# Kernel tuning notes

Hardware: AMD Instinct MI355X
Metric: run time of the kernel (lower is better)

The kernel has to match this reference:

```python
import jax, jax.numpy as jnp
import numpy as np

T, NNODES, DEG = 32, 10000, 32
IN_DIM, H1, HEADS, H2, GRU, PH = 128, 32, 4, 32, 32, 5


def setup_inputs() -> dict:
    key = jax.random.key(0)
    ks = jax.random.split(key, 24)
    d = {}
    d["h"] = jax.random.normal(ks[0], (T, NNODES, IN_DIM), jnp.float32)
    d["src"] = jax.random.randint(ks[1], (NNODES, DEG), 0, NNODES, dtype=jnp.int32)
    d["N"] = jnp.ones((1,), jnp.float32)
    d["I"] = jax.random.uniform(ks[2], (T,), jnp.float32)
    d["R"] = jax.random.uniform(ks[3], (T,), jnp.float32)
    d["S"] = jax.random.uniform(ks[4], (T,), jnp.float32)
    d["It"] = jax.random.uniform(ks[5], (T,), jnp.float32)
    d["Rt"] = jax.random.uniform(ks[6], (T,), jnp.float32)
    d["hx0"] = jax.random.normal(ks[7], (1, GRU), jnp.float32)
    # layer1: HEADS independent GATLayers (fc no-bias, attn_fc no-bias)
    d["W1"] = jax.random.normal(ks[8], (HEADS, IN_DIM, H1), jnp.float32) / np.sqrt(IN_DIM)
    d["a1"] = jax.random.normal(ks[9], (HEADS, 2 * H1), jnp.float32) / np.sqrt(2 * H1)
    # layer2: single head over concatenated features
    d["W2"] = jax.random.normal(ks[10], (1, HEADS * H1, H2), jnp.float32) / np.sqrt(HEADS * H1)
    d["a2"] = jax.random.normal(ks[11], (1, 2 * H2), jnp.float32) / np.sqrt(2 * H2)
    # GRUCell params (torch layout: W_ih [3*gru, in], W_hh [3*gru, gru])
    sg = 1.0 / np.sqrt(GRU)
    d["W_ih"] = jax.random.normal(ks[12], (3 * GRU, H2), jnp.float32) * sg
    d["W_hh"] = jax.random.normal(ks[13], (3 * GRU, GRU), jnp.float32) * sg
    d["b_ih"] = jax.random.normal(ks[14], (3 * GRU,), jnp.float32) * sg
    d["b_hh"] = jax.random.normal(ks[15], (3 * GRU,), jnp.float32) * sg
    sr = 1.0 / np.sqrt(GRU + 2)
    d["Wr1"] = jax.random.normal(ks[16], (2 * PH, GRU + 2), jnp.float32) * sr
    d["br1"] = jax.random.normal(ks[17], (2 * PH,), jnp.float32) * sr
    d["Wr2"] = jax.random.normal(ks[18], (2, GRU + 2), jnp.float32) * sr
    d["br2"] = jax.random.normal(ks[19], (2,), jnp.float32) * sr
    return d


def _gat(x, W, a, src):
    # x: [n, din]; W: [H, din, dout]; a: [H, 2*dout]; src: [n, D] in-neighbor ids
    dout = W.shape[-1]
    z = jnp.einsum('nd,hde->hne', x, W)                    # [H, n, dout]
    zs = z[:, src]                                          # [H, n, D, dout] mailbox of src feats
    e = (jnp.einsum('hnde,he->hnd', zs, a[:, :dout])        # a . z_src part
         + jnp.einsum('hne,he->hn', z, a[:, dout:])[:, :, None])  # a . z_dst part
    alpha = jax.nn.softmax(jax.nn.leaky_relu(e, 0.01), axis=-1)   # softmax over mailbox dim
    return jnp.einsum('hnd,hnde->hne', alpha, zs)           # [H, n, dout]


def reference(h, src, N, I, R, S, It, Rt, hx0, W1, a1, W2, a2,
              W_ih, W_hh, b_ih, b_hh, Wr1, br1, Wr2, br2):
    n = h.shape[1]
    Ns = N.squeeze()

    def step(hx, xs):
        iz, I_t, R_t, S_t, It_t, Rt_t = xs
        h1 = jax.nn.relu(_gat(iz, W1, a1, src))             # [H, n, H1]
        h1 = jnp.transpose(h1, (1, 0, 2)).reshape(n, -1)    # cat heads -> [n, H*H1]
        h2 = _gat(h1, W2, a2, src)[0]                       # [n, H2]
        cur = jnp.max(jax.nn.relu(h2), axis=0)[None, :]     # [1, H2]
        # GRUCell
        gi = cur @ W_ih.T + b_ih
        gh = hx @ W_hh.T + b_hh
        gir, giz, gin = jnp.split(gi, 3, axis=1)
        ghr, ghz, ghn = jnp.split(gh, 3, axis=1)
        r = jax.nn.sigmoid(gir + ghr)
        zg = jax.nn.sigmoid(giz + ghz)
        ng = jnp.tanh(gin + r * ghn)
        hx_new = (1.0 - zg) * ng + zg * hx                  # [1, GRU]
        new_hx = jnp.concatenate([hx_new, It_t.reshape(1, 1), Rt_t.reshape(1, 1)], axis=1)
        pred = (new_hx @ Wr1.T + br1).squeeze()             # [2*PH]
        ab = (new_hx @ Wr2.T + br2).squeeze()               # [2]
        a_s = jax.nn.sigmoid(ab[0])
        b_s = jax.nn.sigmoid(ab[1])
        new_I_t = pred[0::2]
        new_R_t = pred[1::2]
        # SIR physics rollout with detached recurrence
        last_I, last_R, last_S = I_t, R_t, S_t
        phyI, phyR = [], []
        dI = jnp.zeros(())
        dR = jnp.zeros(())
        for i in range(PH):
            if i > 0:
                last_I = last_I + jax.lax.stop_gradient(dI)
                last_R = last_R + jax.lax.stop_gradient(dR)
                last_S = Ns - last_I - last_R
            dI = a_s * last_I * (last_S / Ns) - b_s * last_I
            dR = b_s * last_I
            phyI.append(dI)
            phyR.append(dR)
        return hx_new, (new_I_t, new_R_t, jnp.stack(phyI), jnp.stack(phyR))

    _, (nI, nR, pI, pR) = jax.lax.scan(step, hx0, (h, I, R, S, It, Rt))
    return nI, nR, pI.reshape(-1), pR.reshape(-1)
```

## Files before the change

### kernel.cpp

```cpp
#include <hip/hip_runtime.h>

typedef __attribute__((ext_vector_type(8))) short short8;
typedef __attribute__((ext_vector_type(4))) float floatx4;
typedef __attribute__((ext_vector_type(2))) float float2v;
typedef __attribute__((ext_vector_type(4))) unsigned int uint4v;
typedef __attribute__((ext_vector_type(4))) int int4v;
typedef __attribute__((ext_vector_type(2))) unsigned int uint2v;

__device__ __forceinline__ float bf2f(unsigned short u) {
    return __uint_as_float(((unsigned int)u) << 16);
}
__device__ __forceinline__ unsigned short f2bf(float f) {
    unsigned int x = __float_as_uint(f);
    unsigned int r = (x + 0x7FFFu + ((x >> 16) & 1u)) >> 16;
    return (unsigned short)r;
}
__device__ __forceinline__ float ldf(const void* p, long i, bool f32) {
    return f32 ? ((const float*)p)[i] : bf2f(((const unsigned short*)p)[i]);
}
__device__ __forceinline__ bool detect_f32(const unsigned short* Nv) {
    return Nv[0] == 0;
}

#define P_WIH 0
#define P_WHH 3072
#define P_BIH 6144
#define P_BHH 6240
#define P_WR1 6336
#define P_BR1 6676
#define P_WR2 6686
#define P_BR2 6754
#define P_I   6756
#define P_R   6788
#define P_S   6820
#define P_IT  6852
#define P_RT  6884
#define P_N   6916
#define P_HX0 6917
#define P_TOT 6949

__global__ __launch_bounds__(256) void norm_params(
    const void* W1, const void* a1, const void* W2, const void* a2,
    const void* W_ih, const void* W_hh, const void* b_ih, const void* b_hh,
    const void* Wr1, const void* br1, const void* Wr2, const void* br2,
    const void* Iv, const void* Rv, const void* Sv, const void* Itv, const void* Rtv,
    const void* Nv, const void* hx0,
    float* __restrict__ P, unsigned short* __restrict__ WbT1,
    unsigned short* __restrict__ WbT2)
{
    bool f32 = detect_f32((const unsigned short*)Nv);
    int tid = threadIdx.x;
    struct Item { const void* p; int n; int off; };
    const Item items[15] = {
        {W_ih, 3072, P_WIH}, {W_hh, 3072, P_WHH}, {b_ih, 96, P_BIH}, {b_hh, 96, P_BHH},
        {Wr1, 340, P_WR1}, {br1, 10, P_BR1}, {Wr2, 68, P_WR2}, {br2, 2, P_BR2},
        {Iv, 32, P_I}, {Rv, 32, P_R}, {Sv, 32, P_S}, {Itv, 32, P_IT}, {Rtv, 32, P_RT},
        {Nv, 1, P_N}, {hx0, 32, P_HX0}
    };
    for (int it = 0; it < 15; it++)
        for (int i = tid; i < items[it].n; i += 256)
            P[items[it].off + i] = ldf(items[it].p, i, f32);

    for (int idx = tid; idx < 144 * 128; idx += 256) {
        int col = idx >> 7, k = idx & 127;
        float v = 0.f;
        if (col < 128) {
            int h = col >> 5, e = col & 31;
            v = ldf(W1, (h * 128 + k) * 32 + e, f32);
        } else if (col < 136) {
            int q = col - 128;
            int h = (q < 4) ? q : q - 4;
            int off = (q < 4) ? 0 : 32;
            float s = 0.f;
            for (int e = 0; e < 32; e++)
                s += ldf(W1, (h * 128 + k) * 32 + e, f32) * ldf(a1, h * 64 + off + e, f32);
            v = s;
        }
        WbT1[col * 128 + k] = f2bf(v);
    }
    for (int idx = tid; idx < 48 * 128; idx += 256) {
        int col = idx >> 7, k = idx & 127;
        float v = 0.f;
        if (col < 32) {
            v = ldf(W2, k * 32 + col, f32);
        } else if (col < 34) {
            int off = (col == 32) ? 0 : 32;
            float s = 0.f;
            for (int e = 0; e < 32; e++)
                s += ldf(W2, k * 32 + e, f32) * ldf(a2, off + e, f32);
            v = s;
        }
        WbT2[col * 128 + k] = f2bf(v);
    }
}

template<int NT, int HC, bool DYN>
__global__ __launch_bounds__(256) void gat_linear(
    const void* __restrict__ Xv, const unsigned short* __restrict__ WbT,
    unsigned short* __restrict__ Z, float* __restrict__ EL, float* __restrict__ ER,
    const unsigned short* __restrict__ Nv, long row0)
{
    constexpr int NCOL = NT * 16;
    constexpr int LDW  = 136;
    __shared__ unsigned short Ws[NCOL * LDW];
    int tid = threadIdx.x;
    for (int idx = tid; idx < NCOL * 16; idx += 256) {
        int col = idx >> 4, ch = idx & 15;
        *(uint4v*)(&Ws[col * LDW + ch * 8]) = *(const uint4v*)(&WbT[col * 128 + ch * 8]);
    }
    __syncthreads();

    bool f32 = DYN ? detect_f32(Nv) : false;
    int wave = tid >> 6, lane = tid & 63;
    int l15 = lane & 15, quad = lane >> 4;
    long lrow = (long)blockIdx.x * 64 + wave * 16;

    floatx4 acc[NT];
    floatx4 zz = {0.f, 0.f, 0.f, 0.f};
    #pragma unroll
    for (int i = 0; i < NT; i++) acc[i] = zz;

    long xoff = (row0 + lrow + l15) * 128 + quad * 8;
    #pragma unroll
    for (int kt = 0; kt < 4; kt++) {
        short8 afrag;
        if (DYN && f32) {
            const float* xr = (const float*)Xv + xoff + kt * 32;
            float4 u0 = ((const float4*)xr)[0];
            float4 u1 = ((const float4*)xr)[1];
            union { short8 v; unsigned short u[8]; } af;
            af.u[0] = f2bf(u0.x); af.u[1] = f2bf(u0.y);
            af.u[2] = f2bf(u0.z); af.u[3] = f2bf(u0.w);
            af.u[4] = f2bf(u1.x); af.u[5] = f2bf(u1.y);
            af.u[6] = f2bf(u1.z); af.u[7] = f2bf(u1.w);
            afrag = af.v;
        } else {
            afrag = *(const short8*)((const unsigned short*)Xv + xoff + kt * 32);
        }
        #pragma unroll
        for (int nt = 0; nt < NT; nt++) {
            short8 bfrag = *(const short8*)(&Ws[(nt * 16 + l15) * LDW + kt * 32 + quad * 8]);
            acc[nt] = __builtin_amdgcn_mfma_f32_16x16x32_bf16(afrag, bfrag, acc[nt], 0, 0, 0);
        }
    }

    #pragma unroll
    for (int nt = 0; nt < NT; nt++) {
        int col = nt * 16 + l15;
        #pragma unroll
        for (int r = 0; r < 4; r++) {
            long grow = lrow + quad * 4 + r;
            float v = acc[nt][r];
            if (col < HC * 32) {
                Z[grow * (HC * 32) + col] = f2bf(v);
            } else if (col < HC * 32 + HC) {
                EL[grow * HC + (col - HC * 32)] = v;
            } else if (col < HC * 32 + 2 * HC) {
                ER[grow * HC + (col - HC * 32 - HC)] = v;
            }
        }
    }
}

__global__ __launch_bounds__(256, 3) void gat1_aggr(
    const int* __restrict__ src,
    const unsigned short* __restrict__ Z,
    const float* __restrict__ EL,
    const float* __restrict__ ER,
    unsigned short* __restrict__ H1,
    int NX)
{
    __shared__ float als[4][8][4][36];
    __shared__ int   sid[4][8][32];
    int tid = threadIdx.x;
    int w = tid >> 6, lane = tid & 63;
    int d31 = lane & 31, g = lane >> 5;
    int fl = lane & 15, q = lane >> 4;
    int h = fl >> 2;

    int bid = blockIdx.x;
    int xcd = bid % NX;
    int j   = bid / NX;
    int tq  = j / 313;
    int r   = j - tq * 313;
    int t   = tq * NX + xcd;
    int tb  = t * 10000;
    int n0  = r * 32 + w * 8;
    const char* Zb = (const char*)Z + (size_t)tb * 256;

    int sidx[8];
    float2v elv[8], erv[8];
    #pragma unroll
    for (int jj = 0; jj < 8; jj++) {
        int n = n0 + jj; n = n > 9999 ? 9999 : n;
        sidx[jj] = src[n * 32 + d31];
    }
    #pragma unroll
    for (int jj = 0; jj < 8; jj++)
        elv[jj] = *(const float2v*)(EL + (size_t)(tb + sidx[jj]) * 4 + g * 2);
    #pragma unroll
    for (int jj = 0; jj < 8; jj++) {
        int n = n0 + jj; n = n > 9999 ? 9999 : n;
        erv[jj] = *(const float2v*)(ER + (size_t)(tb + n) * 4 + g * 2);
    }
    float e0[8], e1[8], m0[8], m1[8];
    #pragma unroll
    for (int jj = 0; jj < 8; jj++) {
        float a = elv[jj][0] + erv[jj][0];
        float b = elv[jj][1] + erv[jj][1];
        e0[jj] = a >= 0.f ? a : 0.01f * a;
        e1[jj] = b >= 0.f ? b : 0.01f * b;
        m0[jj] = e0[jj]; m1[jj] = e1[jj];
    }
    #pragma unroll
    for (int off = 16; off > 0; off >>= 1) {
        #pragma unroll
        for (int jj = 0; jj < 8; jj++) {
            m0[jj] = fmaxf(m0[jj], __shfl_xor(m0[jj], off));
            m1[jj] = fmaxf(m1[jj], __shfl_xor(m1[jj], off));
        }
    }
    float x0[8], x1[8], s0[8], s1[8];
    #pragma unroll
    for (int jj = 0; jj < 8; jj++) {
        x0[jj] = __expf(e0[jj] - m0[jj]);
        x1[jj] = __expf(e1[jj] - m1[jj]);
        s0[jj] = x0[jj]; s1[jj] = x1[jj];
    }
    #pragma unroll
    for (int off = 16; off > 0; off >>= 1) {
        #pragma unroll
        for (int jj = 0; jj < 8; jj++) {
            s0[jj] += __shfl_xor(s0[jj], off);
            s1[jj] += __shfl_xor(s1[jj], off);
        }
    }
    #pragma unroll
    for (int jj = 0; jj < 8; jj++) {
        als[w][jj][2 * g + 0][d31] = x0[jj] / s0[jj];
        als[w][jj][2 * g + 1][d31] = x1[jj] / s1[jj];
        if (g == 0) sid[w][jj][d31] = sidx[jj];
    }
    __builtin_amdgcn_wave_barrier();

    uint4v buf[2][8];
    {
        int4v ia = *(const int4v*)&sid[w][0][q * 8];
        int4v ib = *(const int4v*)&sid[w][0][q * 8 + 4];
        #pragma unroll
        for (int k = 0; k < 4; k++)
            buf[0][k] = *(const uint4v*)(Zb + (unsigned int)(ia[k] * 256 + fl * 16));
        #pragma unroll
        for (int k = 0; k < 4; k++)
            buf[0][4 + k] = *(const uint4v*)(Zb + (unsigned int)(ib[k] * 256 + fl * 16));
    }
    #pragma unroll
    for (int jj = 0; jj < 8; jj++) {
        int pb = jj & 1;
        if (jj < 7) {
            int4v ia = *(const int4v*)&sid[w][jj + 1][q * 8];
            int4v ib = *(const int4v*)&sid[w][jj + 1][q * 8 + 4];
            #pragma unroll
            for (int k = 0; k < 4; k++)
                buf[pb ^ 1][k] = *(const uint4v*)(Zb + (unsigned int)(ia[k] * 256 + fl * 16));
            #pragma unroll
            for (int k = 0; k < 4; k++)
                buf[pb ^ 1][4 + k] = *(const uint4v*)(Zb + (unsigned int)(ib[k] * 256 + fl * 16));
        }
        floatx4 avA = *(const floatx4*)&als[w][jj][h][q * 8];
        floatx4 avB = *(const floatx4*)&als[w][jj][h][q * 8 + 4];
        float2v c[4];
        #pragma unroll
        for (int i = 0; i < 4; i++) c[i] = (float2v){0.f, 0.f};
        #pragma unroll
        for (int k = 0; k < 8; k++) {
            float a = (k < 4) ? avA[k & 3] : avB[k & 3];
            float2v a2 = {a, a};
            uint4v ld = buf[pb][k];
            float2v f0 = {__uint_as_float(ld.x << 16), __uint_as_float(ld.x & 0xffff0000u)};
            float2v f1 = {__uint_as_float(ld.y << 16), __uint_as_float(ld.y & 0xffff0000u)};
            float2v f2 = {__uint_as_float(ld.z << 16), __uint_as_float(ld.z & 0xffff0000u)};
            float2v f3 = {__uint_as_float(ld.w << 16), __uint_as_float(ld.w & 0xffff0000u)};
            c[0] += a2 * f0;
            c[1] += a2 * f1;
            c[2] += a2 * f2;
            c[3] += a2 * f3;
        }
        #pragma unroll
        for (int i = 0; i < 4; i++) {
            c[i][0] += __shfl_xor(c[i][0], 16);
            c[i][1] += __shfl_xor(c[i][1], 16);
            c[i][0] += __shfl_xor(c[i][0], 32);
            c[i][1] += __shfl_xor(c[i][1], 32);
        }
        if (q == 0 && n0 + jj < 10000) {
            uint4v o;
            #pragma unroll
            for (int i = 0; i < 4; i++) {
                float lo = fmaxf(c[i][0], 0.f);
                float hi = fmaxf(c[i][1], 0.f);
                o[i] = (unsigned int)f2bf(lo) | ((unsigned int)f2bf(hi) << 16);
            }
            __builtin_nontemporal_store(o,
                (uint4v*)((char*)H1 + (size_t)(tb + n0 + jj) * 256 + fl * 16));
        }
    }
}

__global__ __launch_bounds__(256, 4) void gat2_aggr(
    const int* __restrict__ src,
    const unsigned short* __restrict__ Z2,
    const float* __restrict__ EL2,
    const float* __restrict__ ER2,
    int* __restrict__ cur, int t0, int NX)
{
    __shared__ float als2[4][8][32];
    __shared__ int bm[32];
    int tid = threadIdx.x, w = tid >> 6, lane = tid & 63;
    int d31 = lane & 31, g = lane >> 5;
    int g3 = lane >> 3, f7 = lane & 7;

    int bid = blockIdx.x;
    int xcd = bid % NX;
    int j   = bid / NX;
    int tq  = j / 157;
    int r   = j - tq * 157;
    int t   = tq * NX + xcd;
    int tb  = t * 10000;
    int n0  = r * 64 + w * 16;
    const char* Zb = (const char*)Z2 + (size_t)tb * 64;

    if (tid < 32) bm[tid] = 0;
    __syncthreads();

    float m4[4] = {0.f, 0.f, 0.f, 0.f};
    #pragma unroll
    for (int b = 0; b < 2; b++) {
        int nb = n0 + b * 8;
        float ev[8];
        #pragma unroll
        for (int jj = 0; jj < 8; jj++) {
            int n = nb + jj;
            bool ok = n < 10000;
            int sidx = ok ? src[n * 32 + d31] : 0;
            float e = ok ? (EL2[tb + sidx] + ER2[tb + n]) : 0.f;
            ev[jj] = e >= 0.f ? e : 0.01f * e;
        }
        float mx[8];
        #pragma unroll
        for (int jj = 0; jj < 8; jj++) mx[jj] = ev[jj];
        #pragma unroll
        for (int off = 16; off > 0; off >>= 1) {
            #pragma unroll
            for (int jj = 0; jj < 8; jj++)
                mx[jj] = fmaxf(mx[jj], __shfl_xor(mx[jj], off));
        }
        float xv[8], sm[8];
        #pragma unroll
        for (int jj = 0; jj < 8; jj++) { xv[jj] = __expf(ev[jj] - mx[jj]); sm[jj] = xv[jj]; }
        #pragma unroll
        for (int off = 16; off > 0; off >>= 1) {
            #pragma unroll
            for (int jj = 0; jj < 8; jj++)
                sm[jj] += __shfl_xor(sm[jj], off);
        }
        if (g == 0) {
            #pragma unroll
            for (int jj = 0; jj < 8; jj++)
                als2[w][jj][d31] = xv[jj] / sm[jj];
        }
        __builtin_amdgcn_wave_barrier();

        #pragma unroll
        for (int jj = 0; jj < 8; jj++) {
            int n = nb + jj;
            if (n >= 10000) continue;
            floatx4 av4 = *(const floatx4*)&als2[w][jj][g3 * 4];
            int4v mv = *(const int4v*)(src + n * 32 + g3 * 4);
            uint2v ldv[4];
            #pragma unroll
            for (int k = 0; k < 4; k++)
                ldv[k] = *(const uint2v*)(Zb + (unsigned int)(mv[k] * 64 + f7 * 8));
            float c0 = 0.f, c1 = 0.f, c2 = 0.f, c3 = 0.f;
            #pragma unroll
            for (int k = 0; k < 4; k++) {
                c0 += av4[k] * __uint_as_float(ldv[k].x << 16);
                c1 += av4[k] * __uint_as_float(ldv[k].x & 0xffff0000u);
                c2 += av4[k] * __uint_as_float(ldv[k].y << 16);
                c3 += av4[k] * __uint_as_float(ldv[k].y & 0xffff0000u);
            }
            #pragma unroll
            for (int off = 8; off <= 32; off <<= 1) {
                c0 += __shfl_xor(c0, off);
                c1 += __shfl_xor(c1, off);
                c2 += __shfl_xor(c2, off);
                c3 += __shfl_xor(c3, off);
            }
            m4[0] = fmaxf(m4[0], c0);
            m4[1] = fmaxf(m4[1], c1);
            m4[2] = fmaxf(m4[2], c2);
            m4[3] = fmaxf(m4[3], c3);
        }
        __builtin_amdgcn_wave_barrier();
    }
    if (lane < 8) {
        #pragma unroll
        for (int i = 0; i < 4; i++)
            atomicMax(&bm[f7 * 4 + i], __float_as_int(m4[i]));
    }
    __syncthreads();
    if (tid < 32) atomicMax(&cur[(t0 + t) * 32 + tid], bm[tid]);
}

__global__ __launch_bounds__(128) void gru_head(
    const float* __restrict__ P, const float* __restrict__ cur,
    void* __restrict__ outv, const unsigned short* __restrict__ Nv)
{
    bool f32 = detect_f32(Nv);
    __shared__ float Whh[96 * 32], giAll[32 * 96];
    __shared__ float hx[32], gh[96], nh[34];
    int tid = threadIdx.x;
    for (int i = tid; i < 96 * 32; i += 128)
        Whh[i] = P[P_WHH + i];
    for (int o = tid; o < 32 * 96; o += 128) {
        int t = o / 96, gg = o - t * 96;
        float s = P[P_BIH + gg];
        for (int k = 0; k < 32; k++)
            s += cur[t * 32 + k] * P[P_WIH + gg * 32 + k];
        giAll[o] = s;
    }
    if (tid < 32) hx[tid] = P[P_HX0 + tid];
    __syncthreads();

    for (int t = 0; t < 32; t++) {
        if (tid < 96) {
            float sh = 0.f;
            for (int k = 0; k < 32; k++)
                sh += hx[k] * Whh[tid * 32 + k];
            gh[tid] = sh + P[P_BHH + tid];
        }
        __syncthreads();
        if (tid < 32) {
            const float* gi = &giAll[t * 96];
            float r  = 1.f / (1.f + __expf(-(gi[tid] + gh[tid])));
            float zg = 1.f / (1.f + __expf(-(gi[32 + tid] + gh[32 + tid])));
            float ng = tanhf(gi[64 + tid] + r * gh[64 + tid]);
            float hv = (1.f - zg) * ng + zg * hx[tid];
            hx[tid] = hv;
            nh[tid] = hv;
            if (tid == 0) { nh[32] = P[P_IT + t]; nh[33] = P[P_RT + t]; }
        }
        __syncthreads();
        if (tid < 10) {
            float s = P[P_BR1 + tid];
            for (int k = 0; k < 34; k++) s += nh[k] * P[P_WR1 + tid * 34 + k];
            int i = tid >> 1;
            int oi = ((tid & 1) == 0) ? (t * 5 + i) : (160 + t * 5 + i);
            if (f32) ((float*)outv)[oi] = s;
            else     ((unsigned short*)outv)[oi] = f2bf(s);
        }
        if (tid == 64) {
            float ab0 = P[P_BR2 + 0], ab1 = P[P_BR2 + 1];
            for (int k = 0; k < 34; k++) {
                ab0 += nh[k] * P[P_WR2 + k];
                ab1 += nh[k] * P[P_WR2 + 34 + k];
            }
            float a_s = 1.f / (1.f + __expf(-ab0));
            float b_s = 1.f / (1.f + __expf(-ab1));
            float Ns = P[P_N];
            float lI = P[P_I + t], lR = P[P_R + t], lS = P[P_S + t];
            float dI = 0.f, dR = 0.f;
            for (int i = 0; i < 5; i++) {
                if (i > 0) { lI += dI; lR += dR; lS = Ns - lI - lR; }
                dI = a_s * lI * (lS / Ns) - b_s * lI;
                dR = b_s * lI;
                if (f32) {
                    ((float*)outv)[320 + t * 5 + i] = dI;
                    ((float*)outv)[480 + t * 5 + i] = dR;
                } else {
                    ((unsigned short*)outv)[320 + t * 5 + i] = f2bf(dI);
                    ((unsigned short*)outv)[480 + t * 5 + i] = f2bf(dR);
                }
            }
        }
        __syncthreads();
    }
}

extern "C" void kernel_launch(void* const* d_in, const int* in_sizes, int n_in,
                              void* d_out, int out_size, void* d_ws, size_t ws_size,
                              hipStream_t stream) {
    const void* h    = d_in[0];
    const int*  src  = (const int*)d_in[1];
    const void* Nv   = d_in[2];
    const void* Iv   = d_in[3];
    const void* Rv   = d_in[4];
    const void* Sv   = d_in[5];
    const void* Itv  = d_in[6];
    const void* Rtv  = d_in[7];
    const void* hx0  = d_in[8];
    const void* W1   = d_in[9];
    const void* a1   = d_in[10];
    const void* W2   = d_in[11];
    const void* a2   = d_in[12];
    const void* W_ih = d_in[13];
    const void* W_hh = d_in[14];
    const void* b_ih = d_in[15];
    const void* b_hh = d_in[16];
    const void* Wr1  = d_in[17];
    const void* br1  = d_in[18];
    const void* Wr2  = d_in[19];
    const void* br2  = d_in[20];
    const unsigned short* Nu = (const unsigned short*)Nv;

    int TC = 4;
    for (int c = 32; c >= 4; c >>= 1) {
        size_t need = (size_t)c * 10000 * (128 * 2 + 128 * 2 + 16 + 16) + (1 << 20);
        if (need <= ws_size) { TC = c; break; }
    }
    long CR = (long)TC * 10000;

    char* ws = (char*)d_ws;
    size_t off = 0;
    auto alloc = [&](size_t b) {
        void* p = ws + off;
        off += (b + 255) & ~(size_t)255;
        return p;
    };
    float*          Pb   = (float*)alloc(P_TOT * 4);
    unsigned short* WbT1 = (unsigned short*)alloc(144 * 128 * 2);
    unsigned short* WbT2 = (unsigned short*)alloc(48 * 128 * 2);
    float*          cur  = (float*)alloc(32 * 32 * 4);
    unsigned short* z1   = (unsigned short*)alloc((size_t)CR * 128 * 2);
    unsigned short* h1   = (unsigned short*)alloc((size_t)CR * 128 * 2);
    float*          el1  = (float*)alloc((size_t)CR * 4 * 4);
    float*          er1  = (float*)alloc((size_t)CR * 4 * 4);
    unsigned short* z2   = z1;
    float*          el2  = el1;
    float*          er2  = er1;

    (void)hipMemsetAsync(cur, 0, 32 * 32 * 4, stream);
    norm_params<<<1, 256, 0, stream>>>(W1, a1, W2, a2, W_ih, W_hh, b_ih, b_hh,
                                       Wr1, br1, Wr2, br2, Iv, Rv, Sv, Itv, Rtv,
                                       Nv, hx0, Pb, WbT1, WbT2);
    int nchunks = 32 / TC;
    int g1 = (int)(CR / 64);
    int NX = TC < 8 ? TC : 8;
    int TQ = TC / NX;
    for (int c = 0; c < nchunks; c++) {
        long row0 = (long)c * CR;
        gat_linear<9, 4, true><<<g1, 256, 0, stream>>>(h, WbT1, z1, el1, er1, Nu, row0);
        gat1_aggr<<<NX * 313 * TQ, 256, 0, stream>>>(src, z1, el1, er1, h1, NX);
        gat_linear<3, 1, false><<<g1, 256, 0, stream>>>(h1, WbT2, z2, el2, er2, Nu, 0);
        gat2_aggr<<<NX * 157 * TQ, 256, 0, stream>>>(src, z2, el2, er2, (int*)cur, c * TC, NX);
    }
    gru_head<<<1, 128, 0, stream>>>(Pb, cur, d_out, Nu);
}
```

Measured before the change: 688.5 us.

## Remap gat1 aggregation to one node per lane group and use DPP reductions

The gat1 aggregation is remapped so each 16-lane group owns one destination node and walks all 32 neighbours itself. This removes the per-node cross-lane shuffle reduction, and the gathers are issued in two alternating batches of eight loads. Softmax max/sum reductions in both GAT aggregation kernels move from shfl_xor to DPP row rotations plus ds_swizzle, and divisions become hardware reciprocals. Output packing uses the native v_cvt_pk_bf16_f32 instruction. The cost is higher register pressure from holding all neighbour ids and weights per lane, and the reciprocal is slightly less accurate.

```diff
diff --git a/kernel.cpp b/kernel.cpp
--- a/kernel.cpp
+++ b/kernel.cpp
@@ -21,6 +21,35 @@
 __device__ __forceinline__ bool detect_f32(const unsigned short* Nv) {
     return Nv[0] == 0;
 }
+
+template<int CTRL>
+__device__ __forceinline__ float dppf(float x) {
+    return __int_as_float(__builtin_amdgcn_update_dpp(
+        0, __float_as_int(x), CTRL, 0xF, 0xF, true));
+}
+__device__ __forceinline__ float swz16(float x) {
+    return __int_as_float(__builtin_amdgcn_ds_swizzle(__float_as_int(x), 0x401F));
+}
+__device__ __forceinline__ float red32max(float x) {
+    x = fmaxf(x, dppf<0x128>(x));
+    x = fmaxf(x, dppf<0x124>(x));
+    x = fmaxf(x, dppf<0x122>(x));
+    x = fmaxf(x, dppf<0x121>(x));
+    return fmaxf(x, swz16(x));
+}
+__device__ __forceinline__ float red32sum(float x) {
+    x += dppf<0x128>(x);
+    x += dppf<0x124>(x);
+    x += dppf<0x122>(x);
+    x += dppf<0x121>(x);
+    return x + swz16(x);
+}
+__device__ __forceinline__ float addx8_dpp(float x) {
+    return x + dppf<0x128>(x);
+}
+
+#define BFLO(u) __uint_as_float((u) << 16)
+#define BFHI(u) __uint_as_float((u) & 0xffff0000u)
 
 #define P_WIH 0
 #define P_WHH 3072
@@ -162,6 +191,29 @@
     }
 }
 
+__device__ __forceinline__ void iss8(uint4v* buf, const int4v sa, const int4v sb,
+                                     const char* Zb, unsigned fb) {
+    #pragma unroll
+    for (int k = 0; k < 4; k++)
+        buf[k] = *(const uint4v*)(Zb + (unsigned)(sa[k] * 256) + fb);
+    #pragma unroll
+    for (int k = 0; k < 4; k++)
+        buf[4 + k] = *(const uint4v*)(Zb + (unsigned)(sb[k] * 256) + fb);
+}
+__device__ __forceinline__ void cons8(const uint4v* buf, const floatx4 ax, const floatx4 ay,
+                                      float2v& c0, float2v& c1, float2v& c2, float2v& c3) {
+    #pragma unroll
+    for (int k = 0; k < 8; k++) {
+        float a = (k < 4) ? ax[k & 3] : ay[k & 3];
+        float2v ap = {a, a};
+        uint4v ld = buf[k];
+        c0 += ap * (float2v){BFLO(ld.x), BFHI(ld.x)};
+        c1 += ap * (float2v){BFLO(ld.y), BFHI(ld.y)};
+        c2 += ap * (float2v){BFLO(ld.z), BFHI(ld.z)};
+        c3 += ap * (float2v){BFLO(ld.w), BFHI(ld.w)};
+    }
+}
+
 __global__ __launch_bounds__(256, 3) void gat1_aggr(
     const int* __restrict__ src,
     const unsigned short* __restrict__ Z,
@@ -175,8 +227,6 @@
     int tid = threadIdx.x;
     int w = tid >> 6, lane = tid & 63;
     int d31 = lane & 31, g = lane >> 5;
-    int fl = lane & 15, q = lane >> 4;
-    int h = fl >> 2;
 
     int bid = blockIdx.x;
     int xcd = bid % NX;
@@ -203,106 +253,84 @@
         int n = n0 + jj; n = n > 9999 ? 9999 : n;
         erv[jj] = *(const float2v*)(ER + (size_t)(tb + n) * 4 + g * 2);
     }
-    float e0[8], e1[8], m0[8], m1[8];
+    float e0[8], e1[8];
     #pragma unroll
     for (int jj = 0; jj < 8; jj++) {
         float a = elv[jj][0] + erv[jj][0];
         float b = elv[jj][1] + erv[jj][1];
         e0[jj] = a >= 0.f ? a : 0.01f * a;
         e1[jj] = b >= 0.f ? b : 0.01f * b;
-        m0[jj] = e0[jj]; m1[jj] = e1[jj];
-    }
-    #pragma unroll
-    for (int off = 16; off > 0; off >>= 1) {
-        #pragma unroll
-        for (int jj = 0; jj < 8; jj++) {
-            m0[jj] = fmaxf(m0[jj], __shfl_xor(m0[jj], off));
-            m1[jj] = fmaxf(m1[jj], __shfl_xor(m1[jj], off));
-        }
-    }
-    float x0[8], x1[8], s0[8], s1[8];
+    }
+    float x0[8], x1[8];
     #pragma unroll
     for (int jj = 0; jj < 8; jj++) {
-        x0[jj] = __expf(e0[jj] - m0[jj]);
-        x1[jj] = __expf(e1[jj] - m1[jj]);
-        s0[jj] = x0[jj]; s1[jj] = x1[jj];
-    }
-    #pragma unroll
-    for (int off = 16; off > 0; off >>= 1) {
-        #pragma unroll
-        for (int jj = 0; jj < 8; jj++) {
-            s0[jj] += __shfl_xor(s0[jj], off);
-            s1[jj] += __shfl_xor(s1[jj], off);
-        }
+        x0[jj] = __expf(e0[jj] - red32max(e0[jj]));
+        x1[jj] = __expf(e1[jj] - red32max(e1[jj]));
     }
     #pragma unroll
     for (int jj = 0; jj < 8; jj++) {
-        als[w][jj][2 * g + 0][d31] = x0[jj] / s0[jj];
-        als[w][jj][2 * g + 1][d31] = x1[jj] / s1[jj];
+        float r0 = __builtin_amdgcn_rcpf(red32sum(x0[jj]));
+        float r1 = __builtin_amdgcn_rcpf(red32sum(x1[jj]));
+        als[w][jj][2 * g + 0][d31] = x0[jj] * r0;
+        als[w][jj][2 * g + 1][d31] = x1[jj] * r1;
         if (g == 0) sid[w][jj][d31] = sidx[jj];
     }
     __builtin_amdgcn_wave_barrier();
 
-    uint4v buf[2][8];
-    {
-        int4v ia = *(const int4v*)&sid[w][0][q * 8];
-        int4v ib = *(const int4v*)&sid[w][0][q * 8 + 4];
-        #pragma unroll
-        for (int k = 0; k < 4; k++)
-            buf[0][k] = *(const uint4v*)(Zb + (unsigned int)(ia[k] * 256 + fl * 16));
-        #pragma unroll
-        for (int k = 0; k < 4; k++)
-            buf[0][4 + k] = *(const uint4v*)(Zb + (unsigned int)(ib[k] * 256 + fl * 16));
-    }
-    #pragma unroll
-    for (int jj = 0; jj < 8; jj++) {
-        int pb = jj & 1;
-        if (jj < 7) {
-            int4v ia = *(const int4v*)&sid[w][jj + 1][q * 8];
-            int4v ib = *(const int4v*)&sid[w][jj + 1][q * 8 + 4];
-            #pragma unroll
-            for (int k = 0; k < 4; k++)
-                buf[pb ^ 1][k] = *(const uint4v*)(Zb + (unsigned int)(ia[k] * 256 + fl * 16));
-            #pragma unroll
-            for (int k = 0; k < 4; k++)
-                buf[pb ^ 1][4 + k] = *(const uint4v*)(Zb + (unsigned int)(ib[k] * 256 + fl * 16));
-        }
-        floatx4 avA = *(const floatx4*)&als[w][jj][h][q * 8];
-        floatx4 avB = *(const floatx4*)&als[w][jj][h][q * 8 + 4];
-        float2v c[4];
-        #pragma unroll
-        for (int i = 0; i < 4; i++) c[i] = (float2v){0.f, 0.f};
-        #pragma unroll
-        for (int k = 0; k < 8; k++) {
-            float a = (k < 4) ? avA[k & 3] : avB[k & 3];
-            float2v a2 = {a, a};
-            uint4v ld = buf[pb][k];
-            float2v f0 = {__uint_as_float(ld.x << 16), __uint_as_float(ld.x & 0xffff0000u)};
-            float2v f1 = {__uint_as_float(ld.y << 16), __uint_as_float(ld.y & 0xffff0000u)};
-            float2v f2 = {__uint_as_float(ld.z << 16), __uint_as_float(ld.z & 0xffff0000u)};
-            float2v f3 = {__uint_as_float(ld.w << 16), __uint_as_float(ld.w & 0xffff0000u)};
-            c[0] += a2 * f0;
-            c[1] += a2 * f1;
-            c[2] += a2 * f2;
-            c[3] += a2 * f3;
-        }
-        #pragma unroll
-        for (int i = 0; i < 4; i++) {
-            c[i][0] += __shfl_xor(c[i][0], 16);
-            c[i][1] += __shfl_xor(c[i][1], 16);
-            c[i][0] += __shfl_xor(c[i][0], 32);
-            c[i][1] += __shfl_xor(c[i][1], 32);
-        }
-        if (q == 0 && n0 + jj < 10000) {
-            uint4v o;
-            #pragma unroll
-            for (int i = 0; i < 4; i++) {
-                float lo = fmaxf(c[i][0], 0.f);
-                float hi = fmaxf(c[i][1], 0.f);
-                o[i] = (unsigned int)f2bf(lo) | ((unsigned int)f2bf(hi) << 16);
-            }
+    int u = lane >> 4;
+    int f = lane & 15;
+    int h = f >> 2;
+    unsigned fb = (unsigned)f * 16u;
+
+    #pragma unroll
+    for (int g4 = 0; g4 < 2; g4++) {
+        int jj = g4 * 4 + u;
+        const int* sp = &sid[w][jj][0];
+        int4v sv0 = *(const int4v*)(sp + 0);
+        int4v sv1 = *(const int4v*)(sp + 4);
+        int4v sv2 = *(const int4v*)(sp + 8);
+        int4v sv3 = *(const int4v*)(sp + 12);
+        int4v sv4 = *(const int4v*)(sp + 16);
+        int4v sv5 = *(const int4v*)(sp + 20);
+        int4v sv6 = *(const int4v*)(sp + 24);
+        int4v sv7 = *(const int4v*)(sp + 28);
+
+        uint4v zA[8], zB[8];
+        iss8(zA, sv0, sv1, Zb, fb);
+        iss8(zB, sv2, sv3, Zb, fb);
+
+        const float* ap_ = &als[w][jj][h][0];
+        floatx4 av0 = *(const floatx4*)(ap_ + 0);
+        floatx4 av1 = *(const floatx4*)(ap_ + 4);
+        floatx4 av2 = *(const floatx4*)(ap_ + 8);
+        floatx4 av3 = *(const floatx4*)(ap_ + 12);
+        floatx4 av4 = *(const floatx4*)(ap_ + 16);
+        floatx4 av5 = *(const floatx4*)(ap_ + 20);
+        floatx4 av6 = *(const floatx4*)(ap_ + 24);
+        floatx4 av7 = *(const floatx4*)(ap_ + 28);
+
+        float2v c0 = {0.f, 0.f}, c1 = {0.f, 0.f}, c2 = {0.f, 0.f}, c3 = {0.f, 0.f};
+        cons8(zA, av0, av1, c0, c1, c2, c3);
+        iss8(zA, sv4, sv5, Zb, fb);
+        cons8(zB, av2, av3, c0, c1, c2, c3);
+        iss8(zB, sv6, sv7, Zb, fb);
+        cons8(zA, av4, av5, c0, c1, c2, c3);
+        cons8(zB, av6, av7, c0, c1, c2, c3);
+
+        int n = n0 + jj;
+        if (n < 10000) {
+            float p0 = fmaxf(c0[0], 0.f), p1 = fmaxf(c0[1], 0.f);
+            float p2 = fmaxf(c1[0], 0.f), p3 = fmaxf(c1[1], 0.f);
+            float p4 = fmaxf(c2[0], 0.f), p5 = fmaxf(c2[1], 0.f);
+            float p6 = fmaxf(c3[0], 0.f), p7 = fmaxf(c3[1], 0.f);
+            unsigned r0, r1, r2, r3;
+            asm("v_cvt_pk_bf16_f32 %0, %1, %2" : "=v"(r0) : "v"(p0), "v"(p1));
+            asm("v_cvt_pk_bf16_f32 %0, %1, %2" : "=v"(r1) : "v"(p2), "v"(p3));
+            asm("v_cvt_pk_bf16_f32 %0, %1, %2" : "=v"(r2) : "v"(p4), "v"(p5));
+            asm("v_cvt_pk_bf16_f32 %0, %1, %2" : "=v"(r3) : "v"(p6), "v"(p7));
+            uint4v o = {r0, r1, r2, r3};
             __builtin_nontemporal_store(o,
-                (uint4v*)((char*)H1 + (size_t)(tb + n0 + jj) * 256 + fl * 16));
+                (uint4v*)((char*)H1 + (size_t)(tb + n) * 256 + fb));
         }
     }
 }
@@ -346,28 +374,17 @@
             float e = ok ? (EL2[tb + sidx] + ER2[tb + n]) : 0.f;
             ev[jj] = e >= 0.f ? e : 0.01f * e;
         }
-        float mx[8];
-        #pragma unroll
-        for (int jj = 0; jj < 8; jj++) mx[jj] = ev[jj];
-        #pragma unroll
-        for (int off = 16; off > 0; off >>= 1) {
-            #pragma unroll
-            for (int jj = 0; jj < 8; jj++)
-                mx[jj] = fmaxf(mx[jj], __shfl_xor(mx[jj], off));
-        }
         float xv[8], sm[8];
         #pragma unroll
-        for (int jj = 0; jj < 8; jj++) { xv[jj] = __expf(ev[jj] - mx[jj]); sm[jj] = xv[jj]; }
-        #pragma unroll
-        for (int off = 16; off > 0; off >>= 1) {
-            #pragma unroll
-            for (int jj = 0; jj < 8; jj++)
-                sm[jj] += __shfl_xor(sm[jj], off);
-        }
+        for (int jj = 0; jj < 8; jj++)
+            xv[jj] = __expf(ev[jj] - red32max(ev[jj]));
+        #pragma unroll
+        for (int jj = 0; jj < 8; jj++)
+            sm[jj] = red32sum(xv[jj]);
         if (g == 0) {
             #pragma unroll
             for (int jj = 0; jj < 8; jj++)
-                als2[w][jj][d31] = xv[jj] / sm[jj];
+                als2[w][jj][d31] = xv[jj] * __builtin_amdgcn_rcpf(sm[jj]);
         }
         __builtin_amdgcn_wave_barrier();
 
@@ -389,13 +406,14 @@
                 c2 += av4[k] * __uint_as_float(ldv[k].y << 16);
                 c3 += av4[k] * __uint_as_float(ldv[k].y & 0xffff0000u);
             }
-            #pragma unroll
-            for (int off = 8; off <= 32; off <<= 1) {
-                c0 += __shfl_xor(c0, off);
-                c1 += __shfl_xor(c1, off);
-                c2 += __shfl_xor(c2, off);
-                c3 += __shfl_xor(c3, off);
-            }
+            c0 = addx8_dpp(c0); c1 = addx8_dpp(c1);
+            c2 = addx8_dpp(c2); c3 = addx8_dpp(c3);
+            c0 += swz16(c0); c1 += swz16(c1);
+            c2 += swz16(c2); c3 += swz16(c3);
+            c0 += __shfl_xor(c0, 32);
+            c1 += __shfl_xor(c1, 32);
+            c2 += __shfl_xor(c2, 32);
+            c3 += __shfl_xor(c3, 32);
             m4[0] = fmaxf(m4[0], c0);
             m4[1] = fmaxf(m4[1], c1);
             m4[2] = fmaxf(m4[2], c2);
```

Result: faster. 664.2 us (-3.5%).
